# Optimization experiments

Measured on AMD Instinct MI355X. Metric: run time of the kernel, lower is better.

The kernel has to match this reference:

```python
import jax, jax.numpy as jnp
import numpy as np


def setup_inputs() -> dict:
    key = jax.random.key(0)
    k1, k2, k3, k4 = jax.random.split(key, 4)
    B, S, D_in, D_out = 4, 4096, 768, 64
    x = jax.random.normal(k1, (B, S, D_in), dtype=jnp.float32)
    # torch nn.Linear stores weight as [out, in]; scale to keep activations sane
    scale = 1.0 / np.sqrt(D_in)
    Wq = jax.random.normal(k2, (D_out, D_in), dtype=jnp.float32) * scale
    Wk = jax.random.normal(k3, (D_out, D_in), dtype=jnp.float32) * scale
    Wv = jax.random.normal(k4, (D_out, D_in), dtype=jnp.float32) * scale
    return {"x": x, "Wq": Wq, "Wk": Wk, "Wv": Wv}


def reference(x, Wq, Wk, Wv):
    # q,k,v: [B,S,D_out] via x @ W.T (torch Linear semantics)
    q = jnp.einsum('bsd,od->bso', x, Wq)
    k = jnp.einsum('bsd,od->bso', x, Wk)
    v = jnp.einsum('bsd,od->bso', x, Wv)
    d_out = k.shape[-1]
    scores = jnp.einsum('bqo,bko->bqk', q, k) / jnp.sqrt(jnp.asarray(d_out, x.dtype))
    weights = jax.nn.softmax(scores, axis=-1)  # [B,S,S]
    return jnp.einsum('bqk,bko->bqo', weights, v)
```

## Files before the change

### kernel.cpp

```cpp
#include <hip/hip_runtime.h>
#include <hip/hip_bf16.h>


typedef __attribute__((ext_vector_type(8))) __bf16 bf16x8;
typedef __attribute__((ext_vector_type(4))) __bf16 bf16x4;
typedef __attribute__((ext_vector_type(4))) float  f32x4;

constexpr int BATCH = 4;
constexpr int SEQ   = 4096;
constexpr int DIN   = 768;
constexpr int NTOT  = 192;
constexpr int MROWS = BATCH * SEQ;
constexpr int KVT   = 128;

__device__ __forceinline__ f32x4 mfma16(bf16x8 a, bf16x8 b, f32x4 c) {
    return __builtin_amdgcn_mfma_f32_16x16x32_bf16(a, b, c, 0, 0, 0);
}

__device__ __forceinline__ void gload_lds16(const void* g, void* l) {
    __builtin_amdgcn_global_load_lds(
        (const __attribute__((address_space(1))) void*)g,
        (__attribute__((address_space(3))) void*)l, 16, 0, 0);
}

__global__ __launch_bounds__(256) void convert_w(
        const float* __restrict__ Wq, const float* __restrict__ Wk,
        const float* __restrict__ Wv, __bf16* __restrict__ wb) {
    int i = blockIdx.x * 256 + threadIdx.x;
    if (i >= NTOT * DIN) return;
    int n = i / DIN;
    const float* src = (n < 64) ? Wq : (n < 128) ? Wk : Wv;
    float scale = (n < 64) ? 0.125f * 1.44269504f : 1.0f;
    wb[i] = (__bf16)(src[(n & 63) * DIN + (i % DIN)] * scale);
}

__global__ __launch_bounds__(512, 2) void qkv_proj(
        const float* __restrict__ x, const __bf16* __restrict__ wb,
        __bf16* __restrict__ q, __bf16* __restrict__ k, __bf16* __restrict__ vT) {
    const int tid  = threadIdx.x;
    const int wave = tid >> 6, lane = tid & 63;
    const int strip = wave & 3, nh = wave >> 2;
    const int lr = lane & 15;
    const int g  = lane >> 4;
    const int rx = (lr & 7) << 4;

    __shared__ __align__(16) char wbuf[3][NTOT * 128];
    __shared__ __align__(16) char xbuf[4][64 * 256];

    const int  srow = lane >> 3;
    const int  ssw  = ((lane & 7) << 4) ^ ((srow & 7) << 4);
    const int  xs4  = lane >> 4;
    const char* wbb = (const char*)wb;
    const char* xbb = (const char*)x;
    const int  xrow0 = blockIdx.x * 64;

    auto stage_w = [&](int buf, int kt) {
#pragma unroll
        for (int s = 0; s < 3; ++s) {
            const int rbase = wave * 24 + s * 8;
            gload_lds16(wbb + (size_t)(rbase + srow) * (DIN * 2) + kt * 128 + ssw,
                        &wbuf[buf][rbase * 128]);
        }
    };
    auto stage_x = [&](int buf, int kt) {
#pragma unroll
        for (int s = 0; s < 2; ++s) {
            const int xr = wave * 8 + s * 4;
            const int sswx = ((lane & 15) ^ ((xr & 15) + xs4)) << 4;
            gload_lds16(xbb + (size_t)(xrow0 + xr + xs4) * (DIN * 4) +
                            kt * 256 + sswx,
                        &xbuf[buf][xr * 256]);
        }
    };

    f32x4 acc[6];
#pragma unroll
    for (int t = 0; t < 6; ++t) acc[t] = f32x4{0.f, 0.f, 0.f, 0.f};

    stage_w(0, 0);
    stage_x(0, 0);
    stage_x(1, 1);
    asm volatile("s_waitcnt vmcnt(2) lgkmcnt(0)" ::: "memory");
    __builtin_amdgcn_s_barrier();

    constexpr int NT = DIN / 64;
    for (int kt = 0; kt < NT; ++kt) {
        stage_w((kt + 1) % 3, (kt + 1) % NT);
        stage_x((kt + 2) & 3, (kt + 2) % NT);
        asm volatile("s_waitcnt vmcnt(7) lgkmcnt(0)" ::: "memory");
        __builtin_amdgcn_s_barrier();

        const char* wbc = wbuf[kt % 3];
        const char* xbc = xbuf[kt & 3];
#pragma unroll
        for (int ks = 0; ks < 2; ++ks) {
            const char* xrp = xbc + (strip * 16 + lr) * 256;
            f32x4 xa = *(const f32x4*)(xrp + ((ks * 128 + g * 32)      ^ (lr << 4)));
            f32x4 xb = *(const f32x4*)(xrp + ((ks * 128 + g * 32 + 16) ^ (lr << 4)));
            bf16x8 af;
            af[0] = (__bf16)xa[0]; af[1] = (__bf16)xa[1]; af[2] = (__bf16)xa[2]; af[3] = (__bf16)xa[3];
            af[4] = (__bf16)xb[0]; af[5] = (__bf16)xb[1]; af[6] = (__bf16)xb[2]; af[7] = (__bf16)xb[3];
#pragma unroll
            for (int t = 0; t < 6; ++t) {
                const int nr = (nh * 6 + t) * 16 + lr;
                bf16x8 bf = *(const bf16x8*)(wbc + nr * 128 +
                                             ((ks * 64 + g * 16) ^ rx));
                acc[t] = mfma16(af, bf, acc[t]);
            }
        }
    }

    const int orow = blockIdx.x * 64 + strip * 16 + g * 4;
#pragma unroll
    for (int t = 0; t < 6; ++t) {
        int n = (nh * 6 + t) * 16 + lr;
#pragma unroll
        for (int r = 0; r < 4; ++r) {
            int m = orow + r;
            __bf16 hv = (__bf16)acc[t][r];
            if (n < 64) {
                q[(size_t)m * 64 + n] = hv;
            } else if (n < 128) {
                k[(size_t)m * 64 + (n - 64)] = hv;
            } else {
                int b = m >> 12, s = m & (SEQ - 1);
                vT[(size_t)b * 64 * SEQ + (size_t)(n - 128) * SEQ + s] = hv;
            }
        }
    }
}

__global__ __launch_bounds__(1024, 4) void attn(
        const __bf16* __restrict__ q, const __bf16* __restrict__ k,
        const __bf16* __restrict__ vT, float* __restrict__ out) {
    const int tid  = threadIdx.x;
    const int wave = tid >> 6, lane = tid & 63;
    const int strip = wave & 3, par = wave >> 2;
    const int b  = blockIdx.y;
    const int q0 = blockIdx.x * 64 + strip * 16;
    const int lr = lane & 15;
    const int g  = lane >> 4;
    const int lk = g * 8;
    const int rx = (lr & 7) << 4;

    const __bf16* qp = q  + (size_t)b * SEQ * 64;
    const __bf16* kp = k  + (size_t)b * SEQ * 64;
    const __bf16* vp = vT + (size_t)b * 64 * SEQ;

    __shared__ __align__(16) char kbuf[3][KVT * 128];
    __shared__ __align__(16) char vbuf[3][64 * 256];
    __shared__ __align__(16) char pbuf[16][2048];
    char* pw = &pbuf[wave][0];

    const int  srow8 = lane >> 3;
    const int  sswK  = ((lane & 7) << 4) ^ ((srow8 & 7) << 4);
    const int  vrow  = wave * 4 + (lane >> 4);
    const int  sswV  = ((lane & 15) ^ (vrow & 7)) << 4;

    auto stage = [&](int buf, int kv0) {
        gload_lds16((const char*)kp + (size_t)(kv0 + wave * 8 + srow8) * 128 + sswK,
                    &kbuf[buf][wave * 8 * 128]);
        gload_lds16((const char*)vp + (size_t)vrow * (SEQ * 2) +
                        (size_t)kv0 * 2 + sswV,
                    &vbuf[buf][wave * 4 * 256]);
    };

    bf16x8 qf0 = *(const bf16x8*)(qp + (size_t)(q0 + lr) * 64 + lk);
    bf16x8 qf1 = *(const bf16x8*)(qp + (size_t)(q0 + lr) * 64 + 32 + lk);

    f32x4 acc_o[4];
#pragma unroll
    for (int t = 0; t < 4; ++t) acc_o[t] = f32x4{0.f, 0.f, 0.f, 0.f};
    float l_run = 0.f;

    stage(0, 0);
    asm volatile("s_waitcnt vmcnt(0) lgkmcnt(0)" ::: "memory");
    __builtin_amdgcn_s_barrier();

    constexpr int NT = SEQ / KVT;
    int cur = 0, nxt = 1;
    for (int it = 0; it < NT; ++it) {
        stage(nxt, ((it + 1) & (NT - 1)) * KVT);
        asm volatile("s_waitcnt vmcnt(2) lgkmcnt(0)" ::: "memory");
        __builtin_amdgcn_s_barrier();

        f32x4 s4[2];
#pragma unroll
        for (int j = 0; j < 2; ++j) {
            const char* kr = &kbuf[cur][(par * 32 + j * 16 + lr) * 128];
            bf16x8 kf0 = *(const bf16x8*)(kr + ((g * 16) ^ rx));
            bf16x8 kf1 = *(const bf16x8*)(kr + ((64 + g * 16) ^ rx));
            f32x4 a = f32x4{0.f, 0.f, 0.f, 0.f};
            a = mfma16(kf0, qf0, a);
            a = mfma16(kf1, qf1, a);
            s4[j] = a;
        }

#pragma unroll
        for (int j = 0; j < 2; ++j) {
            bf16x4 pbv;
#pragma unroll
            for (int r = 0; r < 4; ++r) {
                float p = __builtin_amdgcn_exp2f(s4[j][r]);
                l_run += p;
                pbv[r] = (__bf16)p;
            }
            *(bf16x4*)(pw + lr * 128 + ((j * 32 + g * 8) ^ rx)) = pbv;
        }
        asm volatile("s_waitcnt lgkmcnt(0)" ::: "memory");

        bf16x8 pf = *(const bf16x8*)(pw + lr * 128 + ((g * 16) ^ rx));
#pragma unroll
        for (int t = 0; t < 4; ++t) {
            const char* vr = &vbuf[cur][(t * 16 + lr) * 256];
            bf16x8 vf = *(const bf16x8*)(vr + ((par * 64 + g * 16) ^ rx));
            acc_o[t] = mfma16(vf, pf, acc_o[t]);
        }

        cur = nxt; nxt = (nxt == 2) ? 0 : nxt + 1;
    }

    l_run += __shfl_xor(l_run, 16);
    l_run += __shfl_xor(l_run, 32);
    __syncthreads();

    float* mo = (float*)(&kbuf[0][0]);
    float* ml = (float*)(&vbuf[0][0]);
    if (par > 0) {
        const int pi = par - 1;
        float* dst = mo + (size_t)((pi * 4 + strip) * 16 + lr) * 64;
#pragma unroll
        for (int t = 0; t < 4; ++t)
            *(f32x4*)(dst + t * 16 + g * 4) = acc_o[t];
        if (lane < 16) ml[(pi * 4 + strip) * 16 + lr] = l_run;
    }
    __syncthreads();
    if (par == 0) {
        float L = l_run;
#pragma unroll
        for (int pi = 0; pi < 3; ++pi) L += ml[(pi * 4 + strip) * 16 + lr];
        float inv = 1.f / L;
        float* ob = out + ((size_t)b * SEQ + q0 + lr) * 64;
#pragma unroll
        for (int t = 0; t < 4; ++t) {
            f32x4 o4 = acc_o[t];
#pragma unroll
            for (int pi = 0; pi < 3; ++pi)
                o4 += *(const f32x4*)(mo + (size_t)((pi * 4 + strip) * 16 + lr) * 64 +
                                      t * 16 + g * 4);
#pragma unroll
            for (int r = 0; r < 4; ++r) o4[r] *= inv;
            *(f32x4*)(ob + t * 16 + g * 4) = o4;
        }
    }
}

extern "C" void kernel_launch(void* const* d_in, const int* in_sizes, int n_in,
                              void* d_out, int out_size, void* d_ws, size_t ws_size,
                              hipStream_t stream) {
    const float* x  = (const float*)d_in[0];
    const float* Wq = (const float*)d_in[1];
    const float* Wk = (const float*)d_in[2];
    const float* Wv = (const float*)d_in[3];
    float* out = (float*)d_out;

    char* ws = (char*)d_ws;
    __bf16* wb = (__bf16*)(ws);
    __bf16* qb = (__bf16*)(ws + 294912);
    __bf16* kb = (__bf16*)(ws + 294912 + 2097152);
    __bf16* vT = (__bf16*)(ws + 294912 + 2u * 2097152);

    convert_w<<<dim3((NTOT * DIN + 255) / 256), dim3(256), 0, stream>>>(Wq, Wk, Wv, wb);
    qkv_proj<<<dim3(MROWS / 64), dim3(512), 0, stream>>>(x, wb, qb, kb, vT);
    attn<<<dim3(SEQ / 64, BATCH), dim3(1024), 0, stream>>>(qb, kb, vT, out);
}
```

Measured before the change: 54.62 us.

## Restructure attention waves to skip P LDS round-trip via K16 MFMA register layout

Adds a new attention kernel, used when the 16x16x16 bf16 MFMA builtin exists. Each wave now handles two 16-row query strips and a 16-key slice across 8 key partitions. The exp'd score tile stays in registers and feeds the PV MFMA directly in the K16 operand layout, which removes the LDS write/read of P and its waitcnt. The partial outputs from the 8 partitions are combined with a three-step tree reduction through reused LDS. In exchange it uses more accumulator registers and more barriers in the epilogue, and runs twice as many smaller K16 MFMAs for PV.

Result: slower. 58.54 us (+7.2%).

```diff
diff --git a/kernel.cpp b/kernel.cpp
--- a/kernel.cpp
+++ b/kernel.cpp
@@ -5,6 +5,7 @@
 typedef __attribute__((ext_vector_type(8))) __bf16 bf16x8;
 typedef __attribute__((ext_vector_type(4))) __bf16 bf16x4;
 typedef __attribute__((ext_vector_type(4))) float  f32x4;
+typedef __attribute__((ext_vector_type(4))) short  s16x4;
 
 constexpr int BATCH = 4;
 constexpr int SEQ   = 4096;
@@ -13,9 +14,23 @@
 constexpr int MROWS = BATCH * SEQ;
 constexpr int KVT   = 128;
 
+#if defined(__has_builtin)
+#if __has_builtin(__builtin_amdgcn_mfma_f32_16x16x16bf16_1k)
+#define HAVE_MFMA_K16 1
+#endif
+#endif
+#ifndef HAVE_MFMA_K16
+#define HAVE_MFMA_K16 0
+#endif
+
 __device__ __forceinline__ f32x4 mfma16(bf16x8 a, bf16x8 b, f32x4 c) {
     return __builtin_amdgcn_mfma_f32_16x16x32_bf16(a, b, c, 0, 0, 0);
 }
+#if HAVE_MFMA_K16
+__device__ __forceinline__ f32x4 mfma16k16(s16x4 a, s16x4 b, f32x4 c) {
+    return __builtin_amdgcn_mfma_f32_16x16x16bf16_1k(a, b, c, 0, 0, 0);
+}
+#endif
 
 __device__ __forceinline__ void gload_lds16(const void* g, void* l) {
     __builtin_amdgcn_global_load_lds(
@@ -130,6 +145,158 @@
     }
 }
 
+#if HAVE_MFMA_K16
+__global__ __launch_bounds__(1024, 4) void attn(
+        const __bf16* __restrict__ q, const __bf16* __restrict__ k,
+        const __bf16* __restrict__ vT, float* __restrict__ out) {
+    const int tid  = threadIdx.x;
+    const int wave = tid >> 6, lane = tid & 63;
+    const int strip = wave & 1, par = wave >> 1;
+    const int b  = blockIdx.y;
+    const int q0 = blockIdx.x * 64 + strip * 32;
+    const int lr = lane & 15;
+    const int g  = lane >> 4;
+    const int lk = g * 8;
+    const int rx = (lr & 7) << 4;
+
+    const __bf16* qp = q  + (size_t)b * SEQ * 64;
+    const __bf16* kp = k  + (size_t)b * SEQ * 64;
+    const __bf16* vp = vT + (size_t)b * 64 * SEQ;
+
+    __shared__ __align__(16) char kbuf[3][KVT * 128];
+    __shared__ __align__(16) char vbuf[3][64 * 256];
+    __shared__ float lbuf[8][2][2][16];
+
+    const int  srow8 = lane >> 3;
+    const int  sswK  = ((lane & 7) << 4) ^ ((srow8 & 7) << 4);
+    const int  vrow  = wave * 4 + (lane >> 4);
+    const int  sswV  = ((lane & 15) ^ (vrow & 7)) << 4;
+
+    auto stage = [&](int buf, int kv0) {
+        gload_lds16((const char*)kp + (size_t)(kv0 + wave * 8 + srow8) * 128 + sswK,
+                    &kbuf[buf][wave * 8 * 128]);
+        gload_lds16((const char*)vp + (size_t)vrow * (SEQ * 2) +
+                        (size_t)kv0 * 2 + sswV,
+                    &vbuf[buf][wave * 4 * 256]);
+    };
+
+    bf16x8 qf[2][2];
+#pragma unroll
+    for (int qh = 0; qh < 2; ++qh)
+#pragma unroll
+        for (int ks = 0; ks < 2; ++ks)
+            qf[qh][ks] = *(const bf16x8*)(qp + (size_t)(q0 + qh * 16 + lr) * 64 +
+                                          ks * 32 + lk);
+
+    f32x4 acc[2][4];
+#pragma unroll
+    for (int qh = 0; qh < 2; ++qh)
+#pragma unroll
+        for (int t = 0; t < 4; ++t) acc[qh][t] = f32x4{0.f, 0.f, 0.f, 0.f};
+    float l_run[2] = {0.f, 0.f};
+
+    stage(0, 0);
+    asm volatile("s_waitcnt vmcnt(0) lgkmcnt(0)" ::: "memory");
+    __builtin_amdgcn_s_barrier();
+
+    constexpr int NT = SEQ / KVT;
+    int cur = 0, nxt = 1;
+    for (int it = 0; it < NT; ++it) {
+        stage(nxt, ((it + 1) & (NT - 1)) * KVT);
+        asm volatile("s_waitcnt vmcnt(2) lgkmcnt(0)" ::: "memory");
+        __builtin_amdgcn_s_barrier();
+
+        const char* kr = &kbuf[cur][(par * 16 + lr) * 128];
+        bf16x8 kf0 = *(const bf16x8*)(kr + ((g * 16) ^ rx));
+        bf16x8 kf1 = *(const bf16x8*)(kr + ((64 + g * 16) ^ rx));
+
+        s16x4 pb[2];
+#pragma unroll
+        for (int qh = 0; qh < 2; ++qh) {
+            f32x4 a = f32x4{0.f, 0.f, 0.f, 0.f};
+            a = mfma16(kf0, qf[qh][0], a);
+            a = mfma16(kf1, qf[qh][1], a);
+#pragma unroll
+            for (int r = 0; r < 4; ++r) {
+                float p = __builtin_amdgcn_exp2f(a[r]);
+                l_run[qh] += p;
+                pb[qh][r] = __builtin_bit_cast(short, (__bf16)p);
+            }
+        }
+
+#pragma unroll
+        for (int t = 0; t < 4; ++t) {
+            const char* vr = &vbuf[cur][(t * 16 + lr) * 256];
+            s16x4 vf = *(const s16x4*)(vr + ((par * 32 + g * 8) ^ rx));
+#pragma unroll
+            for (int qh = 0; qh < 2; ++qh)
+                acc[qh][t] = mfma16k16(vf, pb[qh], acc[qh][t]);
+        }
+
+        cur = nxt; nxt = (nxt == 2) ? 0 : nxt + 1;
+    }
+
+#pragma unroll
+    for (int qh = 0; qh < 2; ++qh) {
+        l_run[qh] += __shfl_xor(l_run[qh], 16);
+        l_run[qh] += __shfl_xor(l_run[qh], 32);
+    }
+    if (lane < 16) {
+        lbuf[par][strip][0][lr] = l_run[0];
+        lbuf[par][strip][1][lr] = l_run[1];
+    }
+    __syncthreads();
+
+    auto regp = [&](int r) -> float* {
+        return (r < 6) ? ((float*)&kbuf[0][0] + (size_t)r * 2048)
+                       : ((float*)&vbuf[0][0] + (size_t)(r - 6) * 2048);
+    };
+    auto publish = [&](float* dst) {
+#pragma unroll
+        for (int qh = 0; qh < 2; ++qh)
+#pragma unroll
+            for (int t = 0; t < 4; ++t)
+                *(f32x4*)(dst + (lr * 2 + qh) * 64 + t * 16 + g * 4) = acc[qh][t];
+    };
+    auto absorb = [&](const float* src) {
+#pragma unroll
+        for (int qh = 0; qh < 2; ++qh)
+#pragma unroll
+            for (int t = 0; t < 4; ++t)
+                acc[qh][t] += *(const f32x4*)(src + (lr * 2 + qh) * 64 +
+                                              t * 16 + g * 4);
+    };
+
+    if (par >= 4) publish(regp((par - 4) * 2 + strip));
+    __syncthreads();
+    if (par < 4) absorb(regp(par * 2 + strip));
+    __syncthreads();
+    if (par == 2 || par == 3) publish(regp((par - 2) * 2 + strip));
+    __syncthreads();
+    if (par < 2) absorb(regp(par * 2 + strip));
+    __syncthreads();
+    if (par == 1) publish(regp(strip));
+    __syncthreads();
+    if (par == 0) {
+        absorb(regp(strip));
+#pragma unroll
+        for (int qh = 0; qh < 2; ++qh) {
+            float L = 0.f;
+#pragma unroll
+            for (int p = 0; p < 8; ++p) L += lbuf[p][strip][qh][lr];
+            float inv = 1.f / L;
+            float* ob = out + ((size_t)b * SEQ + q0 + qh * 16 + lr) * 64;
+#pragma unroll
+            for (int t = 0; t < 4; ++t) {
+                f32x4 o4 = acc[qh][t];
+#pragma unroll
+                for (int r = 0; r < 4; ++r) o4[r] *= inv;
+                *(f32x4*)(ob + t * 16 + g * 4) = o4;
+            }
+        }
+    }
+}
+#else
 __global__ __launch_bounds__(1024, 4) void attn(
         const __bf16* __restrict__ q, const __bf16* __restrict__ k,
         const __bf16* __restrict__ vT, float* __restrict__ out) {
@@ -195,7 +362,6 @@
             a = mfma16(kf1, qf1, a);
             s4[j] = a;
         }
-
 #pragma unroll
         for (int j = 0; j < 2; ++j) {
             bf16x4 pbv;
@@ -254,6 +420,7 @@
         }
     }
 }
+#endif
 
 extern "C" void kernel_launch(void* const* d_in, const int* in_sizes, int n_in,
                               void* d_out, int out_size, void* d_ws, size_t ws_size,
```
